# Kernel optimization log

Hardware: AMD Instinct MI355X
Metric: run time of the kernel (lower is better)

## Reference

```python
import jax, jax.numpy as jnp
from jax import lax
import numpy as np

N = 17          # num_joints
HID = 64        # hidden_dim
EPS = 1e-5      # BatchNorm eps
SKELETON_CONNECTIONS = [(0, 1), (0, 2), (1, 3), (2, 4), (5, 7), (7, 9), (6, 8), (8, 10), (5, 6), (5, 11), (6, 12), (11, 13), (13, 15), (12, 14), (14, 16), (11, 12)]


def _build_adj():
    a = np.zeros((N, N), dtype=np.float32)
    np.fill_diagonal(a, 1.0)
    for i, j in SKELETON_CONNECTIONS:
        a[i, j] = 1.0
        a[j, i] = 1.0
    dinv = 1.0 / np.sqrt(a.sum(1))
    return jnp.asarray(a * dinv[:, None] * dinv[None, :])

ADJ = _build_adj()  # [N, N], D^-1/2 (A+I) D^-1/2


def _bn(x, g, b):
    # eval-mode BatchNorm1d with running_mean=0, running_var=1; x: [B, C, T]
    s = g / jnp.sqrt(1.0 + EPS)
    return x * s[None, :, None] + b[None, :, None]


def _gconv1d(x, w, b, groups, pad):
    # grouped temporal conv; x: [B, C, T], w: [Cout, Cin//groups, K]
    y = lax.conv_general_dilated(x, w, (1,), [(pad, pad)], feature_group_count=groups,
                                 dimension_numbers=('NCH', 'OIH', 'NCH'))
    return y + b[None, :, None]


def _block(x, gw, gb, bn1g, bn1b, cw, cb, bn2g, bn2b, res):
    # STGCNBlock; x: [B, T, N, Cin]
    B, T, n, Cin = x.shape
    Cout = gw.shape[1]
    xr = x.reshape(B, T, n * Cin).transpose(0, 2, 1)  # [B, n*Cin, T]
    if res is None:
        r = xr
    else:
        rw, rb, rg, rbb = res
        r = _bn(_gconv1d(xr, rw, rb, n, 0), rg, rbb)
    # GCN applied to all timesteps at once (replaces the per-t python loop):
    # support = x @ W ; out = adj @ support + bias
    y = jnp.einsum('mn,btno->btmo', ADJ, jnp.einsum('btni,io->btno', x, gw)) + gb
    h = y.reshape(B, T, n * Cout).transpose(0, 2, 1)  # [B, n*Cout, T]
    h = jax.nn.relu(_bn(h, bn1g, bn1b))
    h = _gconv1d(h, cw, cb, n, 1)                    # k=3, pad=1, groups=N
    h = jax.nn.relu(_bn(h, bn2g, bn2b))              # dropout is identity (eval)
    out = h + r
    return out.transpose(0, 2, 1).reshape(B, T, n, Cout)


def setup_inputs() -> dict:
    key = jax.random.key(0)
    ks = iter(jax.random.split(key, 64))

    def rn(shape, scale=0.05):
        return (scale * jax.random.normal(next(ks), shape)).astype(jnp.float32)

    B, T = 64, 512
    C = 2 * HID  # 128
    inp = {'x': jax.random.normal(next(ks), (B, T, N * 3), dtype=jnp.float32)}
    inp['w_in'] = rn((HID, 3))
    inp['b_in'] = rn((HID,))
    for i, cin in enumerate([HID, C, C]):
        inp[f'gw{i}'] = rn((cin, C))
        inp[f'gb{i}'] = rn((C,))
        inp[f'bn1g{i}'] = 1.0 + rn((N * C,))
        inp[f'bn1b{i}'] = rn((N * C,))
        inp[f'cw{i}'] = rn((N * C, C, 3))
        inp[f'cb{i}'] = rn((N * C,))
        inp[f'bn2g{i}'] = 1.0 + rn((N * C,))
        inp[f'bn2b{i}'] = rn((N * C,))
    inp['rw0'] = rn((N * C, HID, 1))
    inp['rb0'] = rn((N * C,))
    inp['rg0'] = 1.0 + rn((N * C,))
    inp['rbb0'] = rn((N * C,))
    inp['w1'] = rn((N * C, 128))
    inp['b1'] = rn((128,))
    inp['w2'] = rn((128, 64))
    inp['b2'] = rn((64,))
    inp['w3'] = rn((64, 1))
    inp['b3'] = rn((1,))
    return inp


def reference(x, w_in, b_in, gw0, gb0, bn1g0, bn1b0, cw0, cb0, bn2g0, bn2b0,
              gw1, gb1, bn1g1, bn1b1, cw1, cb1, bn2g1, bn2b1,
              gw2, gb2, bn1g2, bn1b2, cw2, cb2, bn2g2, bn2b2,
              rw0, rb0, rg0, rbb0, w1, b1, w2, b2, w3, b3):
    B, T, F = x.shape
    x4 = x.reshape(B, T, N, F // N)                       # [B,T,N,3]
    h = jnp.einsum('btnc,oc->btno', x4, w_in) + b_in      # Conv1d k=1 input transform
    h = _block(h, gw0, gb0, bn1g0, bn1b0, cw0, cb0, bn2g0, bn2b0, (rw0, rb0, rg0, rbb0))
    h = _block(h, gw1, gb1, bn1g1, bn1b1, cw1, cb1, bn2g1, bn2b1, None)
    h = _block(h, gw2, gb2, bn1g2, bn1b2, cw2, cb2, bn2g2, bn2b2, None)
    h = h.mean(axis=1).reshape(B, -1)                     # temporal mean -> [B, N*2*HID]
    h = jax.nn.relu(h @ w1 + b1)
    h = jax.nn.relu(h @ w2 + b2)
    return jax.nn.sigmoid(h @ w3 + b3)                    # [B, 1]
```

## Files before the change

### kernel.cpp

```cpp
#include <hip/hip_runtime.h>
#include <math.h>

#define BNUM 64
#define TNUM 512
#define NJ   17
#define CC   128
#define HIDC 64

#define RSQ 0.9999950000374997f

typedef __attribute__((ext_vector_type(8))) short bf16x8;
typedef __attribute__((ext_vector_type(4))) float f32x4;

__device__ __forceinline__ float bf2f(unsigned short u) {
    union { unsigned int i; float f; } v; v.i = ((unsigned int)u) << 16; return v.f;
}
__device__ __forceinline__ unsigned short f2bf(float f) {
    union { float f; unsigned int i; } v; v.f = f;
    return (unsigned short)((v.i + 0x7FFF + ((v.i >> 16) & 1)) >> 16);
}

constexpr unsigned ADJM[NJ] = {
    0x7u, 0xBu, 0x15u, 0xAu, 0x14u,
    0x8E0u, 0x1160u, 0x2A0u, 0x540u, 0x280u, 0x500u,
    0x3820u, 0x5840u, 0xA800u, 0x15000u, 0xA000u, 0x14000u
};
constexpr float DINV[NJ] = {
    0.5773502691896258f, 0.5773502691896258f, 0.5773502691896258f,
    0.7071067811865476f, 0.7071067811865476f,
    0.5f, 0.5f,
    0.5773502691896258f, 0.5773502691896258f,
    0.7071067811865476f, 0.7071067811865476f,
    0.5f, 0.5f,
    0.5773502691896258f, 0.5773502691896258f,
    0.7071067811865476f, 0.7071067811865476f
};

__global__ void k_fallback(float* out) { out[threadIdx.x] = 0.f; }

__global__ void k_prep_cwB(const float* __restrict__ cw, unsigned short* __restrict__ cwB) {
    const int idx = blockIdx.x * 256 + threadIdx.x;
    if (idx >= NJ * CC * 3 * CC) return;
    const int oc = idx / 384, kk = idx % 384;
    const int ktap = kk >> 7, i = kk & 127;
    cwB[idx] = f2bf(cw[((size_t)oc * CC + i) * 3 + ktap]);
}
__global__ void k_prep_rwB(const float* __restrict__ rw, unsigned short* __restrict__ rwB) {
    const int idx = blockIdx.x * 256 + threadIdx.x;
    if (idx >= NJ * CC * HIDC) return;
    rwB[idx] = f2bf(rw[idx]);
}
template<int CIN>
__global__ void k_prep_gwB(const float* __restrict__ gw, unsigned short* __restrict__ gwB) {
    const int idx = blockIdx.x * 256 + threadIdx.x;
    if (idx >= CC * CIN) return;
    const int o = idx / CIN, i = idx % CIN;
    gwB[idx] = f2bf(gw[i * CC + o]);
}

template<int CIN>
__device__ __forceinline__ void gcn_mfma_body(
        const unsigned short* __restrict__ gwB,
        const float* __restrict__ gb,
        const float* __restrict__ bn1g, const float* __restrict__ bn1b,
        unsigned short* __restrict__ H1, unsigned short* lds,
        int bt0, int tid) {
    const int lane = tid & 63;
    const int wnt  = tid >> 6;
    const int rbase = lane & 15;
    const int g8    = (lane >> 4) * 8;

    f32x4 acc[17][2] = {};
#pragma unroll
    for (int ks = 0; ks < CIN / 32; ++ks) {
        bf16x8 bfr[2];
#pragma unroll
        for (int nt = 0; nt < 2; ++nt)
            bfr[nt] = *reinterpret_cast<const bf16x8*>(
                &gwB[(size_t)(wnt * 32 + nt * 16 + rbase) * CIN + ks * 32 + g8]);
#pragma unroll
        for (int mt = 0; mt < 17; ++mt) {
            const int rl = mt * 16 + rbase;
            const bf16x8 a = *reinterpret_cast<const bf16x8*>(
                &lds[(rl * CIN + ks * 32 + g8) ^ ((rl & 7) << 3)]);
            acc[mt][0] = __builtin_amdgcn_mfma_f32_16x16x32_bf16(a, bfr[0], acc[mt][0], 0, 0, 0);
            acc[mt][1] = __builtin_amdgcn_mfma_f32_16x16x32_bf16(a, bfr[1], acc[mt][1], 0, 0, 0);
        }
    }
    __syncthreads();

    const int rrow = (lane >> 4) * 4;
#pragma unroll
    for (int mt = 0; mt < 17; ++mt)
#pragma unroll
        for (int nt = 0; nt < 2; ++nt)
#pragma unroll
            for (int q = 0; q < 4; ++q) {
                const int r = mt * 16 + rrow + q;
                const int o = wnt * 32 + nt * 16 + rbase;
                lds[(r * 128 + o) ^ ((r & 7) << 3)] = f2bf(acc[mt][nt][q]);
            }
    __syncthreads();

    const int o    = tid & 127;
    const int half = tid >> 7;
    float gbo[NJ], s1c[NJ], b1c[NJ];
#pragma unroll
    for (int m = 0; m < NJ; ++m) {
        const int ch = m * CC + o;
        gbo[m] = gb[ch];
        s1c[m] = bn1g[ch] * RSQ;
        b1c[m] = bn1b[ch];
    }
    for (int j = 0; j < 8; ++j) {
        const int btl = half * 8 + j;
        float s[NJ];
#pragma unroll
        for (int n = 0; n < NJ; ++n) {
            const int r = btl * NJ + n;
            s[n] = bf2f(lds[(r * 128 + o) ^ ((r & 7) << 3)]) * DINV[n];
        }
        unsigned short outv[NJ];
#pragma unroll
        for (int m = 0; m < NJ; ++m) {
            float ym = 0.f;
#pragma unroll
            for (int n = 0; n < NJ; ++n)
                if (ADJM[m] & (1u << n)) ym += s[n];
            ym = fmaf(ym, DINV[m], gbo[m]);
            outv[m] = f2bf(fmaxf(fmaf(ym, s1c[m], b1c[m]), 0.f));
        }
        unsigned short* hp = &H1[(size_t)(bt0 + btl) * (NJ * CC) + o];
#pragma unroll
        for (int m = 0; m < NJ; ++m) hp[m * CC] = outv[m];
    }
}

__global__ __launch_bounds__(256, 1) void k_gcn_mfma(
        const unsigned short* __restrict__ X, const unsigned short* __restrict__ gwB,
        const float* __restrict__ gb,
        const float* __restrict__ bn1g, const float* __restrict__ bn1b,
        unsigned short* __restrict__ H1) {
    __shared__ __align__(16) unsigned short lds[272 * 128];
    const int bt0 = blockIdx.x * 16;
    const int tid = threadIdx.x;
    for (int c = tid; c < 272 * 16; c += 256) {
        const int rl = c >> 4, s8 = c & 15;
        const uint4 v = *reinterpret_cast<const uint4*>(
            &X[(size_t)(bt0 * NJ + rl) * CC + s8 * 8]);
        *reinterpret_cast<uint4*>(&lds[(rl * 128 + s8 * 8) ^ ((rl & 7) << 3)]) = v;
    }
    __syncthreads();
    gcn_mfma_body<CC>(gwB, gb, bn1g, bn1b, H1, lds, bt0, tid);
}

__global__ __launch_bounds__(256, 1) void k_gcn0_mfma(
        const float* __restrict__ x,
        const float* __restrict__ w_in, const float* __restrict__ b_in,
        const unsigned short* __restrict__ gwB,
        const float* __restrict__ gb,
        const float* __restrict__ bn1g, const float* __restrict__ bn1b,
        unsigned short* __restrict__ H1) {
    __shared__ __align__(16) unsigned short lds[272 * 128];
    const int bt0 = blockIdx.x * 16;
    const int tid = threadIdx.x;
    for (int c = tid; c < 272 * 8; c += 256) {
        const int rl = c >> 3, i8 = c & 7;
        const int bt = bt0 + rl / NJ, n = rl % NJ;
        const float* xb = &x[(size_t)bt * (NJ * 3) + n * 3];
        const float x0 = xb[0], x1 = xb[1], x2 = xb[2];
        unsigned short tmp[8];
#pragma unroll
        for (int jj = 0; jj < 8; ++jj) {
            const int i = i8 * 8 + jj;
            tmp[jj] = f2bf(fmaf(x2, w_in[i * 3 + 2],
                           fmaf(x1, w_in[i * 3 + 1],
                           fmaf(x0, w_in[i * 3 + 0], b_in[i]))));
        }
        *reinterpret_cast<uint4*>(&lds[(rl * HIDC + i8 * 8) ^ ((rl & 7) << 3)]) =
            *reinterpret_cast<uint4*>(tmp);
    }
    __syncthreads();
    gcn_mfma_body<HIDC>(gwB, gb, bn1g, bn1b, H1, lds, bt0, tid);
}

template<int RES_MODE>
__global__ __launch_bounds__(256) void k_tconv_mfma(
        const unsigned short* __restrict__ H1, const unsigned short* __restrict__ cwB,
        const float* __restrict__ cb,
        const float* __restrict__ bn2g, const float* __restrict__ bn2b,
        const float* __restrict__ RSRC,
        const float* __restrict__ w_in, const float* __restrict__ b_in,
        const unsigned short* __restrict__ rwB, const float* __restrict__ rb,
        const float* __restrict__ rg, const float* __restrict__ rbb,
        unsigned short* __restrict__ OUT) {
    __shared__ __align__(16) unsigned short xin[66 * 128];
    __shared__ __align__(16) unsigned short h0s[RES_MODE ? 64 * 64 : 8];

    const int t0  = blockIdx.x * 64;
    const int n   = blockIdx.y;
    const int b   = blockIdx.z;
    const int tid = threadIdx.x;
    const int lane = tid & 63;
    const int wnt  = tid >> 6;

    for (int c = tid; c < 66 * 16; c += 256) {
        const int row = c >> 4, slot = c & 15;
        const int ti = t0 - 1 + row;
        uint4 v = {0u, 0u, 0u, 0u};
        if (ti >= 0 && ti < TNUM)
            v = *reinterpret_cast<const uint4*>(
                    &H1[(((size_t)b * TNUM + ti) * NJ + n) * CC + slot * 8]);
        const int u = (row * 128 + slot * 8) ^ ((row & 7) << 3);
        *reinterpret_cast<uint4*>(&xin[u]) = v;
    }
    if constexpr (RES_MODE == 1) {
        for (int c = tid; c < 64 * 8; c += 256) {
            const int r = c >> 3, i8 = c & 7;
            const float* xb = &RSRC[((size_t)b * TNUM + t0 + r) * (NJ * 3) + n * 3];
            const float x0 = xb[0], x1 = xb[1], x2 = xb[2];
            unsigned short tmp[8];
#pragma unroll
            for (int j = 0; j < 8; ++j) {
                const int i = i8 * 8 + j;
                tmp[j] = f2bf(fmaf(x2, w_in[i * 3 + 2],
                              fmaf(x1, w_in[i * 3 + 1],
                              fmaf(x0, w_in[i * 3 + 0], b_in[i]))));
            }
            const int u = (r * 64 + i8 * 8) ^ ((r & 7) << 3);
            *reinterpret_cast<uint4*>(&h0s[u]) = *reinterpret_cast<uint4*>(tmp);
        }
    }
    __syncthreads();

    const int rbase = lane & 15;
    const int g8    = (lane >> 4) * 8;

    f32x4 acc[4][2] = {};
    for (int ks = 0; ks < 12; ++ks) {
        const int ktap = ks >> 2;
        const int ib   = (ks & 3) * 32 + g8;
        bf16x8 a[4];
#pragma unroll
        for (int m = 0; m < 4; ++m) {
            const int rl = m * 16 + rbase + ktap;
            a[m] = *reinterpret_cast<const bf16x8*>(
                       &xin[(rl * 128 + ib) ^ ((rl & 7) << 3)]);
        }
#pragma unroll
        for (int nt = 0; nt < 2; ++nt) {
            const int o = wnt * 32 + nt * 16 + rbase;
            const bf16x8 bf = *reinterpret_cast<const bf16x8*>(
                &cwB[(size_t)(n * CC + o) * 384 + ks * 32 + g8]);
#pragma unroll
            for (int m = 0; m < 4; ++m)
                acc[m][nt] = __builtin_amdgcn_mfma_f32_16x16x32_bf16(a[m], bf, acc[m][nt], 0, 0, 0);
        }
    }

    f32x4 accr[4][2] = {};
    if constexpr (RES_MODE == 1) {
        for (int ks = 0; ks < 2; ++ks) {
            const int ib = ks * 32 + g8;
            bf16x8 a[4];
#pragma unroll
            for (int m = 0; m < 4; ++m) {
                const int rl = m * 16 + rbase;
                a[m] = *reinterpret_cast<const bf16x8*>(
                           &h0s[(rl * 64 + ib) ^ ((rl & 7) << 3)]);
            }
#pragma unroll
            for (int nt = 0; nt < 2; ++nt) {
                const int o = wnt * 32 + nt * 16 + rbase;
                const bf16x8 bf = *reinterpret_cast<const bf16x8*>(
                    &rwB[(size_t)(n * CC + o) * HIDC + ib]);
#pragma unroll
                for (int m = 0; m < 4; ++m)
                    accr[m][nt] = __builtin_amdgcn_mfma_f32_16x16x32_bf16(a[m], bf, accr[m][nt], 0, 0, 0);
            }
        }
    }

    const int rrow = (lane >> 4) * 4;
#pragma unroll
    for (int nt = 0; nt < 2; ++nt) {
        const int o  = wnt * 32 + nt * 16 + rbase;
        const int ch = n * CC + o;
        const float s2 = bn2g[ch] * RSQ, bb2 = bn2b[ch], cbo = cb[ch];
        float rs = 0.f, rsh = 0.f, rbc = 0.f;
        if constexpr (RES_MODE == 1) { rs = rg[ch] * RSQ; rsh = rbb[ch]; rbc = rb[ch]; }
#pragma unroll
        for (int m = 0; m < 4; ++m) {
#pragma unroll
            for (int q = 0; q < 4; ++q) {
                const int r = m * 16 + rrow + q;
                const size_t oi = (((size_t)b * TNUM + t0 + r) * NJ + n) * CC + o;
                float v = fmaxf(fmaf(acc[m][nt][q] + cbo, s2, bb2), 0.f);
                if constexpr (RES_MODE == 1) v += fmaf(accr[m][nt][q] + rbc, rs, rsh);
                else                         v += bf2f(OUT[oi]);
                OUT[oi] = f2bf(v);
            }
        }
    }
}

__global__ __launch_bounds__(128) void k_pool(const unsigned short* __restrict__ X,
                                              float* __restrict__ P) {
    const int b = blockIdx.x / NJ, n = blockIdx.x % NJ;
    const int o = threadIdx.x;
    const unsigned short* xp = X + ((size_t)b * TNUM * NJ + n) * CC + o;
    float s0 = 0.f, s1 = 0.f, s2 = 0.f, s3 = 0.f;
    for (int t = 0; t < TNUM; t += 4) {
        s0 += bf2f(xp[(size_t)(t + 0) * NJ * CC]);
        s1 += bf2f(xp[(size_t)(t + 1) * NJ * CC]);
        s2 += bf2f(xp[(size_t)(t + 2) * NJ * CC]);
        s3 += bf2f(xp[(size_t)(t + 3) * NJ * CC]);
    }
    P[(size_t)blockIdx.x * CC + o] = (s0 + s1 + s2 + s3) * (1.0f / TNUM);
}

__global__ __launch_bounds__(128) void k_mlp(const float* __restrict__ P,
        const float* __restrict__ w1, const float* __restrict__ b1,
        const float* __restrict__ w2, const float* __restrict__ b2,
        const float* __restrict__ w3, const float* __restrict__ b3,
        float* __restrict__ out) {
    __shared__ float h1[128];
    __shared__ float h2[64];
    const int b = blockIdx.x, tid = threadIdx.x;
    const float* pr = P + (size_t)b * (NJ * CC);
    float acc = b1[tid];
    for (int i = 0; i < NJ * CC; ++i) acc = fmaf(pr[i], w1[i * 128 + tid], acc);
    h1[tid] = fmaxf(acc, 0.f);
    __syncthreads();
    if (tid < 64) {
        float a2 = b2[tid];
#pragma unroll 4
        for (int i = 0; i < 128; ++i) a2 = fmaf(h1[i], w2[i * 64 + tid], a2);
        h2[tid] = fmaxf(a2, 0.f);
    }
    __syncthreads();
    if (tid == 0) {
        float a3 = b3[0];
#pragma unroll 4
        for (int i = 0; i < 64; ++i) a3 = fmaf(h2[i], w3[i], a3);
        out[b] = 1.f / (1.f + expf(-a3));
    }
}

extern "C" void kernel_launch(void* const* d_in, const int* in_sizes, int n_in,
                              void* d_out, int out_size, void* d_ws, size_t ws_size,
                              hipStream_t stream) {
    const float* x    = (const float*)d_in[0];
    const float* w_in = (const float*)d_in[1];
    const float* b_in = (const float*)d_in[2];
    const float *gw[3], *gb[3], *bn1g[3], *bn1b[3], *cw[3], *cb[3], *bn2g[3], *bn2b[3];
    for (int l = 0; l < 3; ++l) {
        const int base = 3 + l * 8;
        gw[l]   = (const float*)d_in[base + 0];
        gb[l]   = (const float*)d_in[base + 1];
        bn1g[l] = (const float*)d_in[base + 2];
        bn1b[l] = (const float*)d_in[base + 3];
        cw[l]   = (const float*)d_in[base + 4];
        cb[l]   = (const float*)d_in[base + 5];
        bn2g[l] = (const float*)d_in[base + 6];
        bn2b[l] = (const float*)d_in[base + 7];
    }
    const float* rw0  = (const float*)d_in[27];
    const float* rb0  = (const float*)d_in[28];
    const float* rg0  = (const float*)d_in[29];
    const float* rbb0 = (const float*)d_in[30];
    const float* w1   = (const float*)d_in[31];
    const float* b1   = (const float*)d_in[32];
    const float* w2   = (const float*)d_in[33];
    const float* b2   = (const float*)d_in[34];
    const float* w3   = (const float*)d_in[35];
    const float* b3   = (const float*)d_in[36];

    const size_t CWB    = (size_t)NJ * CC * 3 * CC;
    const size_t RWB    = (size_t)NJ * CC * HIDC;
    const size_t GWB128 = (size_t)CC * CC;
    const size_t GWB64  = (size_t)CC * HIDC;
    const size_t ACT_B  = (size_t)TNUM * NJ * CC;
    const size_t POOLED = (size_t)BNUM * NJ * CC;
    const size_t fixedB = (3 * CWB + RWB + 2 * GWB128 + GWB64) * sizeof(unsigned short)
                        + POOLED * sizeof(float);

    int chunk = 0;
    for (int c = BNUM; c >= 1; c >>= 1) {
        const size_t need = fixedB + 2 * (size_t)c * ACT_B * sizeof(unsigned short);
        if (need <= ws_size) { chunk = c; break; }
    }
    if (chunk == 0) {
        k_fallback<<<1, 64, 0, stream>>>((float*)d_out);
        return;
    }

    unsigned short* cwB0 = (unsigned short*)d_ws;
    unsigned short* cwB1 = cwB0 + CWB;
    unsigned short* cwB2 = cwB1 + CWB;
    unsigned short* rwB  = cwB2 + CWB;
    unsigned short* gwB0 = rwB + RWB;
    unsigned short* gwB1 = gwB0 + GWB64;
    unsigned short* gwB2 = gwB1 + GWB128;
    float* pooled = (float*)(gwB2 + GWB128);
    unsigned short* bufA = (unsigned short*)(pooled + POOLED);
    unsigned short* bufB = bufA + (size_t)chunk * ACT_B;

    k_prep_cwB<<<(int)((CWB + 255) / 256), 256, 0, stream>>>(cw[0], cwB0);
    k_prep_cwB<<<(int)((CWB + 255) / 256), 256, 0, stream>>>(cw[1], cwB1);
    k_prep_cwB<<<(int)((CWB + 255) / 256), 256, 0, stream>>>(cw[2], cwB2);
    k_prep_rwB<<<(int)((RWB + 255) / 256), 256, 0, stream>>>(rw0, rwB);
    k_prep_gwB<HIDC><<<(int)((GWB64 + 255) / 256), 256, 0, stream>>>(gw[0], gwB0);
    k_prep_gwB<CC><<<(int)((GWB128 + 255) / 256), 256, 0, stream>>>(gw[1], gwB1);
    k_prep_gwB<CC><<<(int)((GWB128 + 255) / 256), 256, 0, stream>>>(gw[2], gwB2);

    for (int b0 = 0; b0 < BNUM; b0 += chunk) {
        const float* xc = x + (size_t)b0 * TNUM * NJ * 3;
        const int GB = chunk * TNUM / 16;
        const dim3 tgrid(TNUM / 64, NJ, chunk);

        k_gcn0_mfma<<<GB, 256, 0, stream>>>(xc, w_in, b_in, gwB0,
                                            gb[0], bn1g[0], bn1b[0], bufA);
        k_tconv_mfma<1><<<tgrid, 256, 0, stream>>>(bufA, cwB0, cb[0], bn2g[0], bn2b[0],
                                                   xc, w_in, b_in, rwB, rb0, rg0, rbb0, bufB);
        k_gcn_mfma<<<GB, 256, 0, stream>>>(bufB, gwB1, gb[1], bn1g[1], bn1b[1], bufA);
        k_tconv_mfma<0><<<tgrid, 256, 0, stream>>>(bufA, cwB1, cb[1], bn2g[1], bn2b[1],
                                                   nullptr, w_in, b_in, nullptr, nullptr, nullptr, nullptr, bufB);
        k_gcn_mfma<<<GB, 256, 0, stream>>>(bufB, gwB2, gb[2], bn1g[2], bn1b[2], bufA);
        k_tconv_mfma<0><<<tgrid, 256, 0, stream>>>(bufA, cwB2, cb[2], bn2g[2], bn2b[2],
                                                   nullptr, w_in, b_in, nullptr, nullptr, nullptr, nullptr, bufB);

        k_pool<<<chunk * NJ, 128, 0, stream>>>(bufB, pooled + (size_t)b0 * NJ * CC);
    }

    k_mlp<<<BNUM, 128, 0, stream>>>(pooled, w1, b1, w2, b2, w3, b3, (float*)d_out);
}
```

Baseline: 1.069 ms.

## Fuse temporal pooling into last tconv and vectorize GCN/tconv epilogues

The temporal mean pooling moves into the final temporal-conv kernel. Each block reduces its 64 timesteps in LDS and atomically adds the result into a zeroed pooled buffer, so the last activation is never written back or re-read by a separate pool kernel. The tconv epilogue now stages results in LDS and does 16-byte vectorized residual reads and writes instead of scalar bf16 accesses. The GCN adjacency epilogue gives each thread 8 channels with uint4 LDS reads and stores. The three conv-weight prep launches are merged into one. Float atomics make the pooled sums order-nondeterministic, and the epilogues add extra LDS barriers.

```diff
diff --git a/kernel.cpp b/kernel.cpp
--- a/kernel.cpp
+++ b/kernel.cpp
@@ -18,6 +18,20 @@
 __device__ __forceinline__ unsigned short f2bf(float f) {
     union { float f; unsigned int i; } v; v.f = f;
     return (unsigned short)((v.i + 0x7FFF + ((v.i >> 16) & 1)) >> 16);
+}
+__device__ __forceinline__ void unpack8(const uint4 v, float* f) {
+    f[0] = bf2f((unsigned short)(v.x & 0xFFFF)); f[1] = bf2f((unsigned short)(v.x >> 16));
+    f[2] = bf2f((unsigned short)(v.y & 0xFFFF)); f[3] = bf2f((unsigned short)(v.y >> 16));
+    f[4] = bf2f((unsigned short)(v.z & 0xFFFF)); f[5] = bf2f((unsigned short)(v.z >> 16));
+    f[6] = bf2f((unsigned short)(v.w & 0xFFFF)); f[7] = bf2f((unsigned short)(v.w >> 16));
+}
+__device__ __forceinline__ uint4 pack8(const float* f) {
+    uint4 v;
+    v.x = (unsigned)f2bf(f[0]) | ((unsigned)f2bf(f[1]) << 16);
+    v.y = (unsigned)f2bf(f[2]) | ((unsigned)f2bf(f[3]) << 16);
+    v.z = (unsigned)f2bf(f[4]) | ((unsigned)f2bf(f[5]) << 16);
+    v.w = (unsigned)f2bf(f[6]) | ((unsigned)f2bf(f[7]) << 16);
+    return v;
 }
 
 constexpr unsigned ADJM[NJ] = {
@@ -37,13 +51,20 @@
 };
 
 __global__ void k_fallback(float* out) { out[threadIdx.x] = 0.f; }
-
-__global__ void k_prep_cwB(const float* __restrict__ cw, unsigned short* __restrict__ cwB) {
+__global__ void k_zero(float* p, int n) {
+    const int i = blockIdx.x * 256 + threadIdx.x;
+    if (i < n) p[i] = 0.f;
+}
+
+__global__ void k_prep_cwB(const float* __restrict__ cw0, const float* __restrict__ cw1,
+                           const float* __restrict__ cw2, unsigned short* __restrict__ cwB) {
     const int idx = blockIdx.x * 256 + threadIdx.x;
     if (idx >= NJ * CC * 3 * CC) return;
+    const float* cw = (blockIdx.y == 0) ? cw0 : (blockIdx.y == 1) ? cw1 : cw2;
     const int oc = idx / 384, kk = idx % 384;
     const int ktap = kk >> 7, i = kk & 127;
-    cwB[idx] = f2bf(cw[((size_t)oc * CC + i) * 3 + ktap]);
+    cwB[(size_t)blockIdx.y * (NJ * CC * 3 * CC) + idx] =
+        f2bf(cw[((size_t)oc * CC + i) * 3 + ktap]);
 }
 __global__ void k_prep_rwB(const float* __restrict__ rw, unsigned short* __restrict__ rwB) {
     const int idx = blockIdx.x * 256 + threadIdx.x;
@@ -102,37 +123,43 @@
             }
     __syncthreads();
 
-    const int o    = tid & 127;
-    const int half = tid >> 7;
-    float gbo[NJ], s1c[NJ], b1c[NJ];
+    const int btl = tid >> 4;
+    const int cg  = tid & 15;
+    float s8[NJ][8];
+#pragma unroll
+    for (int n = 0; n < NJ; ++n) {
+        const int r = btl * NJ + n;
+        const uint4 raw = *reinterpret_cast<const uint4*>(
+            &lds[(r * 128 + cg * 8) ^ ((r & 7) << 3)]);
+        unpack8(raw, s8[n]);
+    }
 #pragma unroll
     for (int m = 0; m < NJ; ++m) {
-        const int ch = m * CC + o;
-        gbo[m] = gb[ch];
-        s1c[m] = bn1g[ch] * RSQ;
-        b1c[m] = bn1b[ch];
-    }
-    for (int j = 0; j < 8; ++j) {
-        const int btl = half * 8 + j;
-        float s[NJ];
+        float ym[8] = {};
 #pragma unroll
         for (int n = 0; n < NJ; ++n) {
-            const int r = btl * NJ + n;
-            s[n] = bf2f(lds[(r * 128 + o) ^ ((r & 7) << 3)]) * DINV[n];
-        }
-        unsigned short outv[NJ];
-#pragma unroll
-        for (int m = 0; m < NJ; ++m) {
-            float ym = 0.f;
-#pragma unroll
-            for (int n = 0; n < NJ; ++n)
-                if (ADJM[m] & (1u << n)) ym += s[n];
-            ym = fmaf(ym, DINV[m], gbo[m]);
-            outv[m] = f2bf(fmaxf(fmaf(ym, s1c[m], b1c[m]), 0.f));
-        }
-        unsigned short* hp = &H1[(size_t)(bt0 + btl) * (NJ * CC) + o];
-#pragma unroll
-        for (int m = 0; m < NJ; ++m) hp[m * CC] = outv[m];
+            if (ADJM[m] & (1u << n)) {
+#pragma unroll
+                for (int j = 0; j < 8; ++j) ym[j] = fmaf(s8[n][j], DINV[n], ym[j]);
+            }
+        }
+        const int ch0 = m * CC + cg * 8;
+        const float4 g0 = *reinterpret_cast<const float4*>(&gb[ch0]);
+        const float4 g1 = *reinterpret_cast<const float4*>(&gb[ch0 + 4]);
+        const float4 a0 = *reinterpret_cast<const float4*>(&bn1g[ch0]);
+        const float4 a1 = *reinterpret_cast<const float4*>(&bn1g[ch0 + 4]);
+        const float4 c0 = *reinterpret_cast<const float4*>(&bn1b[ch0]);
+        const float4 c1 = *reinterpret_cast<const float4*>(&bn1b[ch0 + 4]);
+        const float gbv[8] = {g0.x, g0.y, g0.z, g0.w, g1.x, g1.y, g1.z, g1.w};
+        const float sgv[8] = {a0.x, a0.y, a0.z, a0.w, a1.x, a1.y, a1.z, a1.w};
+        const float sbv[8] = {c0.x, c0.y, c0.z, c0.w, c1.x, c1.y, c1.z, c1.w};
+        float out8[8];
+#pragma unroll
+        for (int j = 0; j < 8; ++j) {
+            const float y = fmaf(ym[j], DINV[m], gbv[j]);
+            out8[j] = fmaxf(fmaf(y, sgv[j] * RSQ, sbv[j]), 0.f);
+        }
+        *reinterpret_cast<uint4*>(&H1[(size_t)(bt0 + btl) * (NJ * CC) + ch0]) = pack8(out8);
     }
 }
 
@@ -184,7 +211,7 @@
     gcn_mfma_body<HIDC>(gwB, gb, bn1g, bn1b, H1, lds, bt0, tid);
 }
 
-template<int RES_MODE>
+template<int RES_MODE, int POOL>
 __global__ __launch_bounds__(256) void k_tconv_mfma(
         const unsigned short* __restrict__ H1, const unsigned short* __restrict__ cwB,
         const float* __restrict__ cb,
@@ -193,7 +220,7 @@
         const float* __restrict__ w_in, const float* __restrict__ b_in,
         const unsigned short* __restrict__ rwB, const float* __restrict__ rb,
         const float* __restrict__ rg, const float* __restrict__ rbb,
-        unsigned short* __restrict__ OUT) {
+        unsigned short* __restrict__ OUT, float* __restrict__ pooled) {
     __shared__ __align__(16) unsigned short xin[66 * 128];
     __shared__ __align__(16) unsigned short h0s[RES_MODE ? 64 * 64 : 8];
 
@@ -281,6 +308,8 @@
         }
     }
 
+    __syncthreads();
+
     const int rrow = (lane >> 4) * 4;
 #pragma unroll
     for (int nt = 0; nt < 2; ++nt) {
@@ -294,29 +323,51 @@
 #pragma unroll
             for (int q = 0; q < 4; ++q) {
                 const int r = m * 16 + rrow + q;
-                const size_t oi = (((size_t)b * TNUM + t0 + r) * NJ + n) * CC + o;
                 float v = fmaxf(fmaf(acc[m][nt][q] + cbo, s2, bb2), 0.f);
                 if constexpr (RES_MODE == 1) v += fmaf(accr[m][nt][q] + rbc, rs, rsh);
-                else                         v += bf2f(OUT[oi]);
-                OUT[oi] = f2bf(v);
-            }
-        }
-    }
-}
-
-__global__ __launch_bounds__(128) void k_pool(const unsigned short* __restrict__ X,
-                                              float* __restrict__ P) {
-    const int b = blockIdx.x / NJ, n = blockIdx.x % NJ;
-    const int o = threadIdx.x;
-    const unsigned short* xp = X + ((size_t)b * TNUM * NJ + n) * CC + o;
-    float s0 = 0.f, s1 = 0.f, s2 = 0.f, s3 = 0.f;
-    for (int t = 0; t < TNUM; t += 4) {
-        s0 += bf2f(xp[(size_t)(t + 0) * NJ * CC]);
-        s1 += bf2f(xp[(size_t)(t + 1) * NJ * CC]);
-        s2 += bf2f(xp[(size_t)(t + 2) * NJ * CC]);
-        s3 += bf2f(xp[(size_t)(t + 3) * NJ * CC]);
-    }
-    P[(size_t)blockIdx.x * CC + o] = (s0 + s1 + s2 + s3) * (1.0f / TNUM);
+                xin[(r * 128 + o) ^ ((r & 7) << 3)] = f2bf(v);
+            }
+        }
+    }
+    __syncthreads();
+
+    float pacc[8] = {};
+    for (int c = tid; c < 64 * 16; c += 256) {
+        const int r = c >> 4, s8 = c & 15;
+        uint4 v = *reinterpret_cast<const uint4*>(
+            &xin[(r * 128 + s8 * 8) ^ ((r & 7) << 3)]);
+        const size_t oi = (((size_t)b * TNUM + t0 + r) * NJ + n) * CC + s8 * 8;
+        if constexpr (RES_MODE == 0) {
+            float f[8], g[8];
+            unpack8(v, f);
+            unpack8(*reinterpret_cast<const uint4*>(&OUT[oi]), g);
+#pragma unroll
+            for (int j = 0; j < 8; ++j) f[j] += g[j];
+            if constexpr (POOL == 1) {
+#pragma unroll
+                for (int j = 0; j < 8; ++j) pacc[j] += f[j];
+            } else {
+                *reinterpret_cast<uint4*>(&OUT[oi]) = pack8(f);
+            }
+        } else {
+            *reinterpret_cast<uint4*>(&OUT[oi]) = v;
+        }
+    }
+
+    if constexpr (POOL == 1) {
+        __syncthreads();
+        float* fred = reinterpret_cast<float*>(xin);
+#pragma unroll
+        for (int j = 0; j < 8; ++j) fred[tid * 8 + j] = pacc[j];
+        __syncthreads();
+        if (tid < 128) {
+            const int s8 = tid >> 3, j = tid & 7;
+            float s = 0.f;
+#pragma unroll
+            for (int k = 0; k < 16; ++k) s += fred[(s8 + 16 * k) * 8 + j];
+            atomicAdd(&pooled[((size_t)b * NJ + n) * CC + s8 * 8 + j], s * (1.0f / TNUM));
+        }
+    }
 }
 
 __global__ __launch_bounds__(128) void k_mlp(const float* __restrict__ P,
@@ -406,31 +457,33 @@
     unsigned short* bufA = (unsigned short*)(pooled + POOLED);
     unsigned short* bufB = bufA + (size_t)chunk * ACT_B;
 
-    k_prep_cwB<<<(int)((CWB + 255) / 256), 256, 0, stream>>>(cw[0], cwB0);
-    k_prep_cwB<<<(int)((CWB + 255) / 256), 256, 0, stream>>>(cw[1], cwB1);
-    k_prep_cwB<<<(int)((CWB + 255) / 256), 256, 0, stream>>>(cw[2], cwB2);
+    dim3 pgrid((int)((CWB + 255) / 256), 3, 1);
+    k_prep_cwB<<<pgrid, 256, 0, stream>>>(cw[0], cw[1], cw[2], cwB0);
     k_prep_rwB<<<(int)((RWB + 255) / 256), 256, 0, stream>>>(rw0, rwB);
     k_prep_gwB<HIDC><<<(int)((GWB64 + 255) / 256), 256, 0, stream>>>(gw[0], gwB0);
     k_prep_gwB<CC><<<(int)((GWB128 + 255) / 256), 256, 0, stream>>>(gw[1], gwB1);
     k_prep_gwB<CC><<<(int)((GWB128 + 255) / 256), 256, 0, stream>>>(gw[2], gwB2);
+    k_zero<<<(int)((POOLED + 255) / 256), 256, 0, stream>>>(pooled, (int)POOLED);
 
     for (int b0 = 0; b0 < BNUM; b0 += chunk) {
         const float* xc = x + (size_t)b0 * TNUM * NJ * 3;
         const int GB = chunk * TNUM / 16;
         const dim3 tgrid(TNUM / 64, NJ, chunk);
+        float* pc = pooled + (size_t)b0 * NJ * CC;
 
         k_gcn0_mfma<<<GB, 256, 0, stream>>>(xc, w_in, b_in, gwB0,
                                             gb[0], bn1g[0], bn1b[0], bufA);
-        k_tconv_mfma<1><<<tgrid, 256, 0, stream>>>(bufA, cwB0, cb[0], bn2g[0], bn2b[0],
-                                                   xc, w_in, b_in, rwB, rb0, rg0, rbb0, bufB);
+        k_tconv_mfma<1, 0><<<tgrid, 256, 0, stream>>>(bufA, cwB0, cb[0], bn2g[0], bn2b[0],
+                                                      xc, w_in, b_in, rwB, rb0, rg0, rbb0,
+                                                      bufB, nullptr);
         k_gcn_mfma<<<GB, 256, 0, stream>>>(bufB, gwB1, gb[1], bn1g[1], bn1b[1], bufA);
-        k_tconv_mfma<0><<<tgrid, 256, 0, stream>>>(bufA, cwB1, cb[1], bn2g[1], bn2b[1],
-                                                   nullptr, w_in, b_in, nullptr, nullptr, nullptr, nullptr, bufB);
+        k_tconv_mfma<0, 0><<<tgrid, 256, 0, stream>>>(bufA, cwB1, cb[1], bn2g[1], bn2b[1],
+                                                      nullptr, w_in, b_in, nullptr, nullptr, nullptr, nullptr,
+                                                      bufB, nullptr);
         k_gcn_mfma<<<GB, 256, 0, stream>>>(bufB, gwB2, gb[2], bn1g[2], bn1b[2], bufA);
-        k_tconv_mfma<0><<<tgrid, 256, 0, stream>>>(bufA, cwB2, cb[2], bn2g[2], bn2b[2],
-                                                   nullptr, w_in, b_in, nullptr, nullptr, nullptr, nullptr, bufB);
-
-        k_pool<<<chunk * NJ, 128, 0, stream>>>(bufB, pooled + (size_t)b0 * NJ * CC);
+        k_tconv_mfma<0, 1><<<tgrid, 256, 0, stream>>>(bufA, cwB2, cb[2], bn2g[2], bn2b[2],
+                                                      nullptr, w_in, b_in, nullptr, nullptr, nullptr, nullptr,
+                                                      bufB, pc);
     }
 
     k_mlp<<<BNUM, 128, 0, stream>>>(pooled, w1, b1, w2, b2, w3, b3, (float*)d_out);
```

New measurement: 1.038 ms. -2.9%, faster.
